# Kernel tuning notes

Hardware: AMD Instinct MI355X
Metric: run time of the kernel (lower is better)

## Reference

```python
import jax, jax.numpy as jnp
import numpy as np

B, S, P, D = 256, 2048, 64, 80

def setup_inputs() -> dict:
    key = jax.random.key(0)
    k1, k2, k3, k4 = jax.random.split(key, 4)
    enc_out = jax.random.normal(k1, (B, S, D), dtype=jnp.float32)
    dec_out = jax.random.normal(k2, (B, P, D), dtype=jnp.float32)
    attn_mask = jax.random.randint(k3, (B, S), 0, 2) > 0  # True = masked
    # guarantee at least one unmasked position per row (avoid NaN softmax)
    attn_mask = attn_mask.at[:, 0].set(False)
    W = jax.random.normal(k4, (D, D), dtype=jnp.float32) * (1.0 / np.sqrt(D))
    return {"enc_out": enc_out, "dec_out": dec_out, "attn_mask": attn_mask, "W": W}

def reference(enc_out, dec_out, attn_mask, W):
    # query = Linear(dec_out) with no bias: y = x @ W^T
    query = jnp.einsum('bpd,ed->bpe', dec_out, W)          # (B, P, D)
    # unscaled attention scores (no 1/sqrt(d) in original)
    weight = jnp.einsum('bpd,bsd->bps', query, enc_out)    # (B, P, S)
    neg = jnp.finfo(weight.dtype).min
    weight = jnp.where(attn_mask[:, None, :], neg, weight)
    weight = jax.nn.softmax(weight, axis=-1)
    context = jnp.einsum('bps,bsd->bpd', weight, enc_out)  # (B, P, D)
    return context
```

## Files before the change

### kernel.cpp

```cpp
#include <hip/hip_runtime.h>

#define NB 256
#define NS 2048
#define NP 64
#define ND 80
#define STILE 128
#define NTILE 16
#define NTHREADS 1024
#define LOG2E 1.4426950408889634f

typedef __attribute__((ext_vector_type(4))) float f32x4;
typedef __attribute__((ext_vector_type(2))) __fp16 fp16x2;
typedef __attribute__((ext_vector_type(8))) _Float16 f16x8;
typedef __attribute__((ext_vector_type(4))) unsigned short u16x4;
typedef unsigned short u16;

#define SMEM_BYTES 60944

__device__ __forceinline__ float E2(float x) { return __builtin_amdgcn_exp2f(x); }
__device__ __forceinline__ unsigned pkh(float lo, float hi) {
  union { fp16x2 h; unsigned u; } cv;
  cv.h = __builtin_amdgcn_cvt_pkrtz(lo, hi);
  return cv.u;
}

__device__ __forceinline__ f32x4 mfma16f(f16x8 a, f16x8 b, f32x4 c) {
  return __builtin_amdgcn_mfma_f32_16x16x32_f16(a, b, c, 0, 0, 0);
}

__global__ __launch_bounds__(NTHREADS, 4)
void DecoderAttention_62989990363717_kernel(const float* __restrict__ enc,
                                            const float* __restrict__ dec,
                                            const int* __restrict__ maskp,
                                            const float* __restrict__ W,
                                            float* __restrict__ out)
{
  __shared__ __align__(16) char smem[SMEM_BYTES];

  u16* ehP    = (u16*)smem;
  float* mbias = (float*)(smem + 50688);
  float* mst  = (float*)(smem + 58880);
  float* lst  = (float*)(smem + 59904);
  int* modep  = (int*)(smem + 60928);

  const int tid  = (int)threadIdx.x;
  const int lane = tid & 63;
  const int wv   = tid >> 6;
  const int pp   = wv & 3;
  const int sq   = wv >> 2;
  const int l15  = lane & 15;
  const int g    = lane >> 4;
  const int b    = (int)blockIdx.x;

  const float* encB = enc + (size_t)b * NS * ND;
  const float* decB = dec + (size_t)b * NP * ND;

  {
    float* Wl = (float*)smem;
    float* dl = (float*)(smem + 26880);
    for (int i = tid; i < 80 * 80; i += NTHREADS) Wl[(i / 80) * 84 + (i % 80)] = W[i];
    for (int i = tid; i < 64 * 80; i += NTHREADS)
      dl[(i / 80) * 84 + (i % 80)] = decB[i] * LOG2E;
    if (tid == 0) {
      const unsigned* mw = (const unsigned*)maskp;
      int ok = 1;
      for (int i = 0; i < 16; ++i) ok &= (mw[i] <= 1u);
      *modep = ok;
    }
    __syncthreads();
    const int m32 = *modep;
    if (m32) {
      int v0 = maskp[(size_t)b * NS + tid];
      int v1 = maskp[(size_t)b * NS + tid + 1024];
      mbias[tid]        = v0 ? -3.0e38f : 0.0f;
      mbias[tid + 1024] = v1 ? -3.0e38f : 0.0f;
    } else if (tid < 512) {
      unsigned w = ((const unsigned*)maskp)[(size_t)b * (NS / 4) + tid];
      f32x4 bb;
      bb[0] = (w & 255u)         ? -3.0e38f : 0.0f;
      bb[1] = ((w >> 8) & 255u)  ? -3.0e38f : 0.0f;
      bb[2] = ((w >> 16) & 255u) ? -3.0e38f : 0.0f;
      bb[3] = (w >> 24)          ? -3.0e38f : 0.0f;
      *(f32x4*)&mbias[4 * tid] = bb;
    }
    float qa[5];
    const int qp = tid & 63, qw = tid >> 6;
#pragma unroll
    for (int j = 0; j < 5; ++j) qa[j] = 0.f;
    for (int kg = 0; kg < 20; ++kg) {
      f32x4 dv = *(const f32x4*)&dl[qp * 84 + kg * 4];
#pragma unroll
      for (int j = 0; j < 5; ++j) {
        f32x4 wv4 = *(const f32x4*)&Wl[(qw * 5 + j) * 84 + kg * 4];
        qa[j] = fmaf(dv.x, wv4.x, qa[j]);
        qa[j] = fmaf(dv.y, wv4.y, qa[j]);
        qa[j] = fmaf(dv.z, wv4.z, qa[j]);
        qa[j] = fmaf(dv.w, wv4.w, qa[j]);
      }
    }
    __syncthreads();
    float* qtmp = (float*)smem;
#pragma unroll
    for (int j = 0; j < 5; ++j) qtmp[qp * 100 + qw * 5 + j] = qa[j];
    if (qw == 15) {
#pragma unroll
      for (int z = 0; z < 16; ++z) qtmp[qp * 100 + 80 + z] = 0.f;
    }
    __syncthreads();
  }

  f16x8 qb[3];
  {
    const float* qtmp = (const float*)smem;
    const int prow = 16 * pp + l15;
#pragma unroll
    for (int kk = 0; kk < 3; ++kk) {
      const int d0 = kk * 32 + g * 8;
      f32x4 f0 = *(const f32x4*)&qtmp[prow * 100 + d0];
      f32x4 f1 = *(const f32x4*)&qtmp[prow * 100 + d0 + 4];
      union { _Float16 h[8]; f16x8 v; } H;
      H.h[0] = (_Float16)f0.x; H.h[1] = (_Float16)f0.y;
      H.h[2] = (_Float16)f0.z; H.h[3] = (_Float16)f0.w;
      H.h[4] = (_Float16)f1.x; H.h[5] = (_Float16)f1.y;
      H.h[6] = (_Float16)f1.z; H.h[7] = (_Float16)f1.w;
      qb[kk] = H.v;
    }
  }
  __syncthreads();

  if (tid < 256) {
    const int buf = tid >> 7, q = (tid >> 4) & 7, row = tid & 15;
    u16* p = ehP + buf * 12672 + (q * 6 + 5) * 264 + row * 16;
    *(uint4*)p = make_uint4(0u, 0u, 0u, 0u);
    *(uint4*)(p + 8) = make_uint4(0u, 0u, 0u, 0u);
  }

  const bool ldr = (tid < 640);
  const int srow = tid / 5;
  const int c    = tid - srow * 5;
  u16* ePW = ehP + ((srow >> 4) * 6 + c) * 264 + (srow & 15) * 16;
  const float* gsrc = encB + srow * ND + 16 * c;

#define STAGE_WRITE(bi)                                                          \
  do {                                                                           \
    if (ldr) {                                                                   \
      unsigned hh[8];                                                            \
      hh[0] = pkh(r0.x, r0.y); hh[1] = pkh(r0.z, r0.w);                          \
      hh[2] = pkh(r1.x, r1.y); hh[3] = pkh(r1.z, r1.w);                          \
      hh[4] = pkh(r2.x, r2.y); hh[5] = pkh(r2.z, r2.w);                          \
      hh[6] = pkh(r3.x, r3.y); hh[7] = pkh(r3.z, r3.w);                          \
      u16* a_ = ePW + (bi) * 12672;                                              \
      *(uint4*)a_       = make_uint4(hh[0], hh[1], hh[2], hh[3]);                \
      *(uint4*)(a_ + 8) = make_uint4(hh[4], hh[5], hh[6], hh[7]);                \
    }                                                                            \
  } while (0)

  {
    f32x4 r0, r1, r2, r3;
    if (ldr) {
      r0 = *(const f32x4*)gsrc;       r1 = *(const f32x4*)(gsrc + 4);
      r2 = *(const f32x4*)(gsrc + 8); r3 = *(const f32x4*)(gsrc + 12);
    }
    STAGE_WRITE(0);
    __syncthreads();
  }

  f32x4 ctx[5];
#pragma unroll
  for (int n = 0; n < 5; ++n) ctx[n] = (f32x4){0.f, 0.f, 0.f, 0.f};
  float mr = -1.0e30f, lr = 0.f;

  const int qkOff = (2 * sq) * 1584 + (g >> 1) * 264 + 16 * l15 + 8 * (g & 1);
  const unsigned trBase = (unsigned)(uintptr_t)ehP + (unsigned)(sq * 6336 + 8 * lane);

  for (int tt = 0; tt < NTILE; ++tt) {
    const int cur = tt & 1, nxt = cur ^ 1;
    const bool hn = (tt + 1 < NTILE);
    f32x4 r0, r1, r2, r3;
    if (hn && ldr) {
      const float* src = gsrc + (size_t)(tt + 1) * STILE * ND;
      r0 = *(const f32x4*)src;       r1 = *(const f32x4*)(src + 4);
      r2 = *(const f32x4*)(src + 8); r3 = *(const f32x4*)(src + 12);
    }

    f32x4 a0 = (f32x4){0.f, 0.f, 0.f, 0.f}, a1 = (f32x4){0.f, 0.f, 0.f, 0.f};
    {
      const u16* baseH0 = ehP + cur * 12672 + qkOff;
      const u16* baseH1 = baseH0 + 1584;
      f16x8 e0[3], e1[3];
#pragma unroll
      for (int kk = 0; kk < 3; ++kk) {
        e0[kk] = *(const f16x8*)(const void*)(baseH0 + kk * 528);
        e1[kk] = *(const f16x8*)(const void*)(baseH1 + kk * 528);
      }
#pragma unroll
      for (int kk = 0; kk < 3; ++kk) {
        a0 = mfma16f(e0[kk], qb[kk], a0);
        a1 = mfma16f(e1[kk], qb[kk], a1);
      }
    }

    const int mb0 = tt * 128 + 32 * sq + 4 * g;
    f32x4 bias0 = *(const f32x4*)&mbias[mb0];
    f32x4 bias1 = *(const f32x4*)&mbias[mb0 + 16];

    const unsigned tra = trBase + (unsigned)(cur * 25344);
    u16x4 ta0, tb0, ta1, tb1, ta2, tb2, ta3, tb3, ta4, tb4;
    asm volatile("ds_read_b64_tr_b16 %0, %1"             : "=v"(ta0) : "v"(tra));
    asm volatile("ds_read_b64_tr_b16 %0, %1 offset:3168" : "=v"(tb0) : "v"(tra));
    asm volatile("ds_read_b64_tr_b16 %0, %1 offset:528"  : "=v"(ta1) : "v"(tra));
    asm volatile("ds_read_b64_tr_b16 %0, %1 offset:3696" : "=v"(tb1) : "v"(tra));
    asm volatile("ds_read_b64_tr_b16 %0, %1 offset:1056" : "=v"(ta2) : "v"(tra));
    asm volatile("ds_read_b64_tr_b16 %0, %1 offset:4224" : "=v"(tb2) : "v"(tra));
    asm volatile("ds_read_b64_tr_b16 %0, %1 offset:1584" : "=v"(ta3) : "v"(tra));
    asm volatile("ds_read_b64_tr_b16 %0, %1 offset:4752" : "=v"(tb3) : "v"(tra));
    asm volatile("ds_read_b64_tr_b16 %0, %1 offset:2112" : "=v"(ta4) : "v"(tra));
    asm volatile("ds_read_b64_tr_b16 %0, %1 offset:5280" : "=v"(tb4) : "v"(tra));

    float sv0[4], sv1[4];
#pragma unroll
    for (int rr = 0; rr < 4; ++rr) {
      sv0[rr] = a0[rr] + bias0[rr];
      sv1[rr] = a1[rr] + bias1[rr];
    }
    float tm = fmaxf(fmaxf(fmaxf(sv0[0], sv0[1]), fmaxf(sv0[2], sv0[3])),
                     fmaxf(fmaxf(sv1[0], sv1[1]), fmaxf(sv1[2], sv1[3])));
    tm = fmaxf(tm, __shfl_xor(tm, 16));
    tm = fmaxf(tm, __shfl_xor(tm, 32));
    const bool need = !__all(tm <= mr + 11.541560f);
    if (need) {
      float mn = fmaxf(mr, tm);
      float esc = E2(mr - mn);
      lr *= esc; mr = mn;
      float fr[4];
#pragma unroll
      for (int rr = 0; rr < 4; ++rr) fr[rr] = __shfl(esc, 4 * g + rr);
#pragma unroll
      for (int n = 0; n < 5; ++n) {
#pragma unroll
        for (int rr = 0; rr < 4; ++rr) ctx[n][rr] *= fr[rr];
      }
    }
    float p0[4], p1[4];
#pragma unroll
    for (int rr = 0; rr < 4; ++rr) {
      p0[rr] = E2(sv0[rr] - mr);
      p1[rr] = E2(sv1[rr] - mr);
    }
    lr += ((p0[0] + p0[1]) + (p0[2] + p0[3])) + ((p1[0] + p1[1]) + (p1[2] + p1[3]));

    union { unsigned uu[4]; f16x8 v; } PA;
    PA.uu[0] = pkh(p0[0], p0[1]); PA.uu[1] = pkh(p0[2], p0[3]);
    PA.uu[2] = pkh(p1[0], p1[1]); PA.uu[3] = pkh(p1[2], p1[3]);
    asm volatile("s_waitcnt lgkmcnt(0)" ::: "memory");
    __builtin_amdgcn_sched_barrier(0);
    {
      union { u16 s[8]; f16x8 v; } B0, B1, B2, B3, B4;
#pragma unroll
      for (int j = 0; j < 4; ++j) {
        B0.s[j] = ta0[j]; B0.s[4 + j] = tb0[j];
        B1.s[j] = ta1[j]; B1.s[4 + j] = tb1[j];
        B2.s[j] = ta2[j]; B2.s[4 + j] = tb2[j];
        B3.s[j] = ta3[j]; B3.s[4 + j] = tb3[j];
        B4.s[j] = ta4[j]; B4.s[4 + j] = tb4[j];
      }
      ctx[0] = mfma16f(PA.v, B0.v, ctx[0]);
      ctx[1] = mfma16f(PA.v, B1.v, ctx[1]);
      ctx[2] = mfma16f(PA.v, B2.v, ctx[2]);
      ctx[3] = mfma16f(PA.v, B3.v, ctx[3]);
      ctx[4] = mfma16f(PA.v, B4.v, ctx[4]);
    }

    if (hn) { STAGE_WRITE(nxt); }
    __syncthreads();
  }

  lr += __shfl_xor(lr, 16);
  lr += __shfl_xor(lr, 32);
  if (g == 0) {
    mst[sq * 64 + 16 * pp + l15] = mr;
    lst[sq * 64 + 16 * pp + l15] = lr;
  }
  __syncthreads();
  float F;
  {
    const int pi = 16 * pp + l15;
    float M = fmaxf(fmaxf(mst[pi], mst[64 + pi]), fmaxf(mst[128 + pi], mst[192 + pi]));
    F = E2(mr - M);
  }
  float gg[4];
#pragma unroll
  for (int rr = 0; rr < 4; ++rr) gg[rr] = __shfl(F, 4 * g + rr);
  float* cacc = (float*)smem;
  for (int qq = 0; qq < 4; ++qq) {
    if (sq == qq) {
#pragma unroll
      for (int n = 0; n < 5; ++n) {
#pragma unroll
        for (int rr = 0; rr < 4; ++rr) {
          const int row = 16 * pp + 4 * g + rr;
          const int col = 16 * n + l15;
          float v = ctx[n][rr] * gg[rr];
          if (qq == 0) cacc[row * 84 + col] = v;
          else         cacc[row * 84 + col] += v;
        }
      }
    }
    __syncthreads();
  }
  {
    const int op = tid >> 4, oc = tid & 15;
    float Mv = fmaxf(fmaxf(mst[op], mst[64 + op]), fmaxf(mst[128 + op], mst[192 + op]));
    float Lv = lst[op] * E2(mst[op] - Mv) + lst[64 + op] * E2(mst[64 + op] - Mv)
             + lst[128 + op] * E2(mst[128 + op] - Mv) + lst[192 + op] * E2(mst[192 + op] - Mv);
    float inv = 1.0f / Lv;
    float* orow = out + ((size_t)b * NP + op) * ND + oc * 5;
    const float* crow = cacc + op * 84 + oc * 5;
#pragma unroll
    for (int i = 0; i < 5; ++i) orow[i] = crow[i] * inv;
  }
}

extern "C" void kernel_launch(void* const* d_in, const int* in_sizes, int n_in,
                              void* d_out, int out_size, void* d_ws, size_t ws_size,
                              hipStream_t stream) {
  (void)in_sizes; (void)n_in; (void)out_size; (void)d_ws; (void)ws_size;
  const float* enc  = (const float*)d_in[0];
  const float* dec  = (const float*)d_in[1];
  const int*   mask = (const int*)d_in[2];
  const float* W    = (const float*)d_in[3];
  float* out = (float*)d_out;
  DecoderAttention_62989990363717_kernel<<<dim3(NB), dim3(NTHREADS), 0, stream>>>(
      enc, dec, mask, W, out);
}
```

Before: 39.89 us.

## Quad-buffer encoder tiles, process two tiles per barrier, use bitmask for attention mask

The staging ring grows from two to four LDS buffers, and each loop iteration handles two 128-row tiles under a single __syncthreads, which halves the number of block barriers. The per-position float mask bias is replaced by a ballot-built bitmask, and masked scores are set to -inf by select instead of an add. LDS use per block rises to about 101 KB, which may limit how many blocks fit per CU. Register pressure also grows from holding two tile bodies per iteration.

Result: slower. 42.14 us (+5.6%).

```diff
diff --git a/kernel.cpp b/kernel.cpp
--- a/kernel.cpp
+++ b/kernel.cpp
@@ -1,13 +1,11 @@
 #include <hip/hip_runtime.h>
 
-#define NB 256
 #define NS 2048
 #define NP 64
 #define ND 80
-#define STILE 128
-#define NTILE 16
 #define NTHREADS 1024
 #define LOG2E 1.4426950408889634f
+#define BUFU 12672
 
 typedef __attribute__((ext_vector_type(4))) float f32x4;
 typedef __attribute__((ext_vector_type(2))) __fp16 fp16x2;
@@ -15,7 +13,7 @@
 typedef __attribute__((ext_vector_type(4))) unsigned short u16x4;
 typedef unsigned short u16;
 
-#define SMEM_BYTES 60944
+#define SMEM_BYTES 103684
 
 __device__ __forceinline__ float E2(float x) { return __builtin_amdgcn_exp2f(x); }
 __device__ __forceinline__ unsigned pkh(float lo, float hi) {
@@ -23,7 +21,6 @@
   cv.h = __builtin_amdgcn_cvt_pkrtz(lo, hi);
   return cv.u;
 }
-
 __device__ __forceinline__ f32x4 mfma16f(f16x8 a, f16x8 b, f32x4 c) {
   return __builtin_amdgcn_mfma_f32_16x16x32_f16(a, b, c, 0, 0, 0);
 }
@@ -37,11 +34,11 @@
 {
   __shared__ __align__(16) char smem[SMEM_BYTES];
 
-  u16* ehP    = (u16*)smem;
-  float* mbias = (float*)(smem + 50688);
-  float* mst  = (float*)(smem + 58880);
-  float* lst  = (float*)(smem + 59904);
-  int* modep  = (int*)(smem + 60928);
+  u16* ehP      = (u16*)smem;
+  unsigned* bitm = (unsigned*)(smem + 101376);
+  float* mst    = (float*)(smem + 101632);
+  float* lst    = (float*)(smem + 102656);
+  int* modep    = (int*)(smem + 103680);
 
   const int tid  = (int)threadIdx.x;
   const int lane = tid & 63;
@@ -51,6 +48,7 @@
   const int l15  = lane & 15;
   const int g    = lane >> 4;
   const int b    = (int)blockIdx.x;
+  const float NEGINF = __uint_as_float(0xFF800000u);
 
   const float* encB = enc + (size_t)b * NS * ND;
   const float* decB = dec + (size_t)b * NP * ND;
@@ -68,20 +66,23 @@
       *modep = ok;
     }
     __syncthreads();
-    const int m32 = *modep;
-    if (m32) {
-      int v0 = maskp[(size_t)b * NS + tid];
-      int v1 = maskp[(size_t)b * NS + tid + 1024];
-      mbias[tid]        = v0 ? -3.0e38f : 0.0f;
-      mbias[tid + 1024] = v1 ? -3.0e38f : 0.0f;
-    } else if (tid < 512) {
-      unsigned w = ((const unsigned*)maskp)[(size_t)b * (NS / 4) + tid];
-      f32x4 bb;
-      bb[0] = (w & 255u)         ? -3.0e38f : 0.0f;
-      bb[1] = ((w >> 8) & 255u)  ? -3.0e38f : 0.0f;
-      bb[2] = ((w >> 16) & 255u) ? -3.0e38f : 0.0f;
-      bb[3] = (w >> 24)          ? -3.0e38f : 0.0f;
-      *(f32x4*)&mbias[4 * tid] = bb;
+    {
+      const int m32 = *modep;
+      int v0, v1;
+      if (m32) {
+        v0 = maskp[(size_t)b * NS + tid] != 0;
+        v1 = maskp[(size_t)b * NS + tid + 1024] != 0;
+      } else {
+        const unsigned char* m8 = (const unsigned char*)maskp;
+        v0 = m8[(size_t)b * NS + tid] != 0;
+        v1 = m8[(size_t)b * NS + tid + 1024] != 0;
+      }
+      unsigned long long b0 = __ballot(v0);
+      unsigned long long b1 = __ballot(v1);
+      if (lane == 0) {
+        *(unsigned long long*)&bitm[2 * wv]      = b0;
+        *(unsigned long long*)&bitm[32 + 2 * wv] = b1;
+      }
     }
     float qa[5];
     const int qp = tid & 63, qw = tid >> 6;
@@ -128,9 +129,9 @@
   }
   __syncthreads();
 
-  if (tid < 256) {
+  if (tid < 512) {
     const int buf = tid >> 7, q = (tid >> 4) & 7, row = tid & 15;
-    u16* p = ehP + buf * 12672 + (q * 6 + 5) * 264 + row * 16;
+    u16* p = ehP + buf * BUFU + (q * 6 + 5) * 264 + row * 16;
     *(uint4*)p = make_uint4(0u, 0u, 0u, 0u);
     *(uint4*)(p + 8) = make_uint4(0u, 0u, 0u, 0u);
   }
@@ -141,27 +142,28 @@
   u16* ePW = ehP + ((srow >> 4) * 6 + c) * 264 + (srow & 15) * 16;
   const float* gsrc = encB + srow * ND + 16 * c;
 
+#define LOAD_T(T)                                                                \
+  do {                                                                           \
+    const float* src = gsrc + (size_t)(T) * 128 * ND;                            \
+    r0 = *(const f32x4*)src;       r1 = *(const f32x4*)(src + 4);                \
+    r2 = *(const f32x4*)(src + 8); r3 = *(const f32x4*)(src + 12);               \
+  } while (0)
+
 #define STAGE_WRITE(bi)                                                          \
   do {                                                                           \
-    if (ldr) {                                                                   \
-      unsigned hh[8];                                                            \
-      hh[0] = pkh(r0.x, r0.y); hh[1] = pkh(r0.z, r0.w);                          \
-      hh[2] = pkh(r1.x, r1.y); hh[3] = pkh(r1.z, r1.w);                          \
-      hh[4] = pkh(r2.x, r2.y); hh[5] = pkh(r2.z, r2.w);                          \
-      hh[6] = pkh(r3.x, r3.y); hh[7] = pkh(r3.z, r3.w);                          \
-      u16* a_ = ePW + (bi) * 12672;                                              \
-      *(uint4*)a_       = make_uint4(hh[0], hh[1], hh[2], hh[3]);                \
-      *(uint4*)(a_ + 8) = make_uint4(hh[4], hh[5], hh[6], hh[7]);                \
-    }                                                                            \
+    unsigned hh[8];                                                              \
+    hh[0] = pkh(r0.x, r0.y); hh[1] = pkh(r0.z, r0.w);                            \
+    hh[2] = pkh(r1.x, r1.y); hh[3] = pkh(r1.z, r1.w);                            \
+    hh[4] = pkh(r2.x, r2.y); hh[5] = pkh(r2.z, r2.w);                            \
+    hh[6] = pkh(r3.x, r3.y); hh[7] = pkh(r3.z, r3.w);                            \
+    u16* a_ = ePW + (bi) * BUFU;                                                 \
+    *(uint4*)a_       = make_uint4(hh[0], hh[1], hh[2], hh[3]);                  \
+    *(uint4*)(a_ + 8) = make_uint4(hh[4], hh[5], hh[6], hh[7]);                  \
   } while (0)
 
   {
     f32x4 r0, r1, r2, r3;
-    if (ldr) {
-      r0 = *(const f32x4*)gsrc;       r1 = *(const f32x4*)(gsrc + 4);
-      r2 = *(const f32x4*)(gsrc + 8); r3 = *(const f32x4*)(gsrc + 12);
-    }
-    STAGE_WRITE(0);
+    if (ldr) { LOAD_T(0); STAGE_WRITE(0); LOAD_T(1); STAGE_WRITE(1); }
     __syncthreads();
   }
 
@@ -172,106 +174,104 @@
 
   const int qkOff = (2 * sq) * 1584 + (g >> 1) * 264 + 16 * l15 + 8 * (g & 1);
   const unsigned trBase = (unsigned)(uintptr_t)ehP + (unsigned)(sq * 6336 + 8 * lane);
-
-  for (int tt = 0; tt < NTILE; ++tt) {
-    const int cur = tt & 1, nxt = cur ^ 1;
-    const bool hn = (tt + 1 < NTILE);
+  const int msh0 = 4 * g, msh1 = 16 + 4 * g;
+
+#define TILE_BODY(TT, BI)                                                        \
+  {                                                                              \
+    const int bO = (BI) * BUFU;                                                  \
+    f32x4 a0 = (f32x4){0.f,0.f,0.f,0.f}, a1 = (f32x4){0.f,0.f,0.f,0.f};          \
+    {                                                                            \
+      const u16* baseH0 = ehP + bO + qkOff;                                      \
+      const u16* baseH1 = baseH0 + 1584;                                         \
+      f16x8 e00 = *(const f16x8*)(const void*)(baseH0);                          \
+      f16x8 e01 = *(const f16x8*)(const void*)(baseH0 + 528);                    \
+      f16x8 e02 = *(const f16x8*)(const void*)(baseH0 + 1056);                   \
+      f16x8 e10 = *(const f16x8*)(const void*)(baseH1);                          \
+      f16x8 e11 = *(const f16x8*)(const void*)(baseH1 + 528);                    \
+      f16x8 e12 = *(const f16x8*)(const void*)(baseH1 + 1056);                   \
+      a0 = mfma16f(e00, qb[0], a0);  a1 = mfma16f(e10, qb[0], a1);               \
+      a0 = mfma16f(e01, qb[1], a0);  a1 = mfma16f(e11, qb[1], a1);               \
+      a0 = mfma16f(e02, qb[2], a0);  a1 = mfma16f(e12, qb[2], a1);               \
+    }                                                                            \
+    const unsigned mw = bitm[4 * (TT) + sq];                                     \
+    const unsigned tra = trBase + (unsigned)(bO * 2);                            \
+    u16x4 ta0, tb0, ta1, tb1, ta2, tb2, ta3, tb3, ta4, tb4;                      \
+    asm volatile("ds_read_b64_tr_b16 %0, %1"             : "=v"(ta0) : "v"(tra));\
+    asm volatile("ds_read_b64_tr_b16 %0, %1 offset:3168" : "=v"(tb0) : "v"(tra));\
+    asm volatile("ds_read_b64_tr_b16 %0, %1 offset:528"  : "=v"(ta1) : "v"(tra));\
+    asm volatile("ds_read_b64_tr_b16 %0, %1 offset:3696" : "=v"(tb1) : "v"(tra));\
+    asm volatile("ds_read_b64_tr_b16 %0, %1 offset:1056" : "=v"(ta2) : "v"(tra));\
+    asm volatile("ds_read_b64_tr_b16 %0, %1 offset:4224" : "=v"(tb2) : "v"(tra));\
+    asm volatile("ds_read_b64_tr_b16 %0, %1 offset:1584" : "=v"(ta3) : "v"(tra));\
+    asm volatile("ds_read_b64_tr_b16 %0, %1 offset:4752" : "=v"(tb3) : "v"(tra));\
+    asm volatile("ds_read_b64_tr_b16 %0, %1 offset:2112" : "=v"(ta4) : "v"(tra));\
+    asm volatile("ds_read_b64_tr_b16 %0, %1 offset:5280" : "=v"(tb4) : "v"(tra));\
+    float sv0[4], sv1[4];                                                        \
+    _Pragma("unroll")                                                            \
+    for (int rr = 0; rr < 4; ++rr) {                                             \
+      sv0[rr] = ((mw >> (msh0 + rr)) & 1u) ? NEGINF : a0[rr];                    \
+      sv1[rr] = ((mw >> (msh1 + rr)) & 1u) ? NEGINF : a1[rr];                    \
+    }                                                                            \
+    float tm = fmaxf(fmaxf(fmaxf(sv0[0], sv0[1]), fmaxf(sv0[2], sv0[3])),        \
+                     fmaxf(fmaxf(sv1[0], sv1[1]), fmaxf(sv1[2], sv1[3])));       \
+    tm = fmaxf(tm, __shfl_xor(tm, 16));                                          \
+    tm = fmaxf(tm, __shfl_xor(tm, 32));                                          \
+    const bool need = !__all(tm <= mr + 11.541560f);                             \
+    if (need) {                                                                  \
+      float mn = fmaxf(mr, tm);                                                  \
+      float esc = E2(mr - mn);                                                   \
+      lr *= esc; mr = mn;                                                        \
+      float fr[4];                                                               \
+      _Pragma("unroll")                                                          \
+      for (int rr = 0; rr < 4; ++rr) fr[rr] = __shfl(esc, 4 * g + rr);           \
+      _Pragma("unroll")                                                          \
+      for (int n = 0; n < 5; ++n) {                                              \
+        _Pragma("unroll")                                                        \
+        for (int rr = 0; rr < 4; ++rr) ctx[n][rr] *= fr[rr];                     \
+      }                                                                          \
+    }                                                                            \
+    float p0[4], p1[4];                                                          \
+    _Pragma("unroll")                                                            \
+    for (int rr = 0; rr < 4; ++rr) {                                             \
+      p0[rr] = E2(sv0[rr] - mr);                                                 \
+      p1[rr] = E2(sv1[rr] - mr);                                                 \
+    }                                                                            \
+    lr += ((p0[0] + p0[1]) + (p0[2] + p0[3])) + ((p1[0] + p1[1]) + (p1[2] + p1[3])); \
+    union { unsigned uu[4]; f16x8 v; } PA;                                       \
+    PA.uu[0] = pkh(p0[0], p0[1]); PA.uu[1] = pkh(p0[2], p0[3]);                  \
+    PA.uu[2] = pkh(p1[0], p1[1]); PA.uu[3] = pkh(p1[2], p1[3]);                  \
+    asm volatile("s_waitcnt lgkmcnt(0)" ::: "memory");                           \
+    __builtin_amdgcn_sched_barrier(0);                                           \
+    {                                                                            \
+      union { u16 s[8]; f16x8 v; } B0, B1, B2, B3, B4;                           \
+      _Pragma("unroll")                                                          \
+      for (int j = 0; j < 4; ++j) {                                              \
+        B0.s[j] = ta0[j]; B0.s[4 + j] = tb0[j];                                  \
+        B1.s[j] = ta1[j]; B1.s[4 + j] = tb1[j];                                  \
+        B2.s[j] = ta2[j]; B2.s[4 + j] = tb2[j];                                  \
+        B3.s[j] = ta3[j]; B3.s[4 + j] = tb3[j];                                  \
+        B4.s[j] = ta4[j]; B4.s[4 + j] = tb4[j];                                  \
+      }                                                                          \
+      ctx[0] = mfma16f(PA.v, B0.v, ctx[0]);                                      \
+      ctx[1] = mfma16f(PA.v, B1.v, ctx[1]);                                      \
+      ctx[2] = mfma16f(PA.v, B2.v, ctx[2]);                                      \
+      ctx[3] = mfma16f(PA.v, B3.v, ctx[3]);                                      \
+      ctx[4] = mfma16f(PA.v, B4.v, ctx[4]);                                      \
+    }                                                                            \
+  }
+
+  for (int kp = 0; kp < 8; ++kp) {
+    const int rb = (kp & 1) << 1;
+    const int wb = 2 - rb;
+    const int tp0 = 2 * kp, tp1 = 2 * kp + 1;
+    const bool h0 = (tp0 + 2 < 16), h1 = (tp1 + 2 < 16);
     f32x4 r0, r1, r2, r3;
-    if (hn && ldr) {
-      const float* src = gsrc + (size_t)(tt + 1) * STILE * ND;
-      r0 = *(const f32x4*)src;       r1 = *(const f32x4*)(src + 4);
-      r2 = *(const f32x4*)(src + 8); r3 = *(const f32x4*)(src + 12);
-    }
-
-    f32x4 a0 = (f32x4){0.f, 0.f, 0.f, 0.f}, a1 = (f32x4){0.f, 0.f, 0.f, 0.f};
-    {
-      const u16* baseH0 = ehP + cur * 12672 + qkOff;
-      const u16* baseH1 = baseH0 + 1584;
-      f16x8 e0[3], e1[3];
-#pragma unroll
-      for (int kk = 0; kk < 3; ++kk) {
-        e0[kk] = *(const f16x8*)(const void*)(baseH0 + kk * 528);
-        e1[kk] = *(const f16x8*)(const void*)(baseH1 + kk * 528);
-      }
-#pragma unroll
-      for (int kk = 0; kk < 3; ++kk) {
-        a0 = mfma16f(e0[kk], qb[kk], a0);
-        a1 = mfma16f(e1[kk], qb[kk], a1);
-      }
-    }
-
-    const int mb0 = tt * 128 + 32 * sq + 4 * g;
-    f32x4 bias0 = *(const f32x4*)&mbias[mb0];
-    f32x4 bias1 = *(const f32x4*)&mbias[mb0 + 16];
-
-    const unsigned tra = trBase + (unsigned)(cur * 25344);
-    u16x4 ta0, tb0, ta1, tb1, ta2, tb2, ta3, tb3, ta4, tb4;
-    asm volatile("ds_read_b64_tr_b16 %0, %1"             : "=v"(ta0) : "v"(tra));
-    asm volatile("ds_read_b64_tr_b16 %0, %1 offset:3168" : "=v"(tb0) : "v"(tra));
-    asm volatile("ds_read_b64_tr_b16 %0, %1 offset:528"  : "=v"(ta1) : "v"(tra));
-    asm volatile("ds_read_b64_tr_b16 %0, %1 offset:3696" : "=v"(tb1) : "v"(tra));
-    asm volatile("ds_read_b64_tr_b16 %0, %1 offset:1056" : "=v"(ta2) : "v"(tra));
-    asm volatile("ds_read_b64_tr_b16 %0, %1 offset:4224" : "=v"(tb2) : "v"(tra));
-    asm volatile("ds_read_b64_tr_b16 %0, %1 offset:1584" : "=v"(ta3) : "v"(tra));
-    asm volatile("ds_read_b64_tr_b16 %0, %1 offset:4752" : "=v"(tb3) : "v"(tra));
-    asm volatile("ds_read_b64_tr_b16 %0, %1 offset:2112" : "=v"(ta4) : "v"(tra));
-    asm volatile("ds_read_b64_tr_b16 %0, %1 offset:5280" : "=v"(tb4) : "v"(tra));
-
-    float sv0[4], sv1[4];
-#pragma unroll
-    for (int rr = 0; rr < 4; ++rr) {
-      sv0[rr] = a0[rr] + bias0[rr];
-      sv1[rr] = a1[rr] + bias1[rr];
-    }
-    float tm = fmaxf(fmaxf(fmaxf(sv0[0], sv0[1]), fmaxf(sv0[2], sv0[3])),
-                     fmaxf(fmaxf(sv1[0], sv1[1]), fmaxf(sv1[2], sv1[3])));
-    tm = fmaxf(tm, __shfl_xor(tm, 16));
-    tm = fmaxf(tm, __shfl_xor(tm, 32));
-    const bool need = !__all(tm <= mr + 11.541560f);
-    if (need) {
-      float mn = fmaxf(mr, tm);
-      float esc = E2(mr - mn);
-      lr *= esc; mr = mn;
-      float fr[4];
-#pragma unroll
-      for (int rr = 0; rr < 4; ++rr) fr[rr] = __shfl(esc, 4 * g + rr);
-#pragma unroll
-      for (int n = 0; n < 5; ++n) {
-#pragma unroll
-        for (int rr = 0; rr < 4; ++rr) ctx[n][rr] *= fr[rr];
-      }
-    }
-    float p0[4], p1[4];
-#pragma unroll
-    for (int rr = 0; rr < 4; ++rr) {
-      p0[rr] = E2(sv0[rr] - mr);
-      p1[rr] = E2(sv1[rr] - mr);
-    }
-    lr += ((p0[0] + p0[1]) + (p0[2] + p0[3])) + ((p1[0] + p1[1]) + (p1[2] + p1[3]));
-
-    union { unsigned uu[4]; f16x8 v; } PA;
-    PA.uu[0] = pkh(p0[0], p0[1]); PA.uu[1] = pkh(p0[2], p0[3]);
-    PA.uu[2] = pkh(p1[0], p1[1]); PA.uu[3] = pkh(p1[2], p1[3]);
-    asm volatile("s_waitcnt lgkmcnt(0)" ::: "memory");
-    __builtin_amdgcn_sched_barrier(0);
-    {
-      union { u16 s[8]; f16x8 v; } B0, B1, B2, B3, B4;
-#pragma unroll
-      for (int j = 0; j < 4; ++j) {
-        B0.s[j] = ta0[j]; B0.s[4 + j] = tb0[j];
-        B1.s[j] = ta1[j]; B1.s[4 + j] = tb1[j];
-        B2.s[j] = ta2[j]; B2.s[4 + j] = tb2[j];
-        B3.s[j] = ta3[j]; B3.s[4 + j] = tb3[j];
-        B4.s[j] = ta4[j]; B4.s[4 + j] = tb4[j];
-      }
-      ctx[0] = mfma16f(PA.v, B0.v, ctx[0]);
-      ctx[1] = mfma16f(PA.v, B1.v, ctx[1]);
-      ctx[2] = mfma16f(PA.v, B2.v, ctx[2]);
-      ctx[3] = mfma16f(PA.v, B3.v, ctx[3]);
-      ctx[4] = mfma16f(PA.v, B4.v, ctx[4]);
-    }
-
-    if (hn) { STAGE_WRITE(nxt); }
+    if (h0 && ldr) LOAD_T(tp0 + 2);
+    TILE_BODY(tp0, rb)
+    if (h0 && ldr) STAGE_WRITE(wb);
+    if (h1 && ldr) LOAD_T(tp1 + 2);
+    TILE_BODY(tp1, rb + 1)
+    if (h1 && ldr) STAGE_WRITE(wb + 1);
     __syncthreads();
   }
 
@@ -330,6 +330,6 @@
   const int*   mask = (const int*)d_in[2];
   const float* W    = (const float*)d_in[3];
   float* out = (float*)d_out;
-  DecoderAttention_62989990363717_kernel<<<dim3(NB), dim3(NTHREADS), 0, stream>>>(
+  DecoderAttention_62989990363717_kernel<<<dim3(256), dim3(NTHREADS), 0, stream>>>(
       enc, dec, mask, W, out);
 }
```
